# Optimization experiments

Measured on AMD Instinct MI355X. Metric: run time of the kernel, lower is better.

Reference implementation:

```python
import jax, jax.numpy as jnp
import numpy as np

B, N, E = 2, 50000, 1000000
F_IN, MSG, F_OUT, EDGE_F = 64, 64, 64, 16

def softsign(v):
    return v / (1.0 + jnp.abs(v))

def setup_inputs() -> dict:
    key = jax.random.key(0)
    ks = jax.random.split(key, 12)
    def w(k, i, o, s=0.02):
        return jax.random.normal(k, (i, o), jnp.float32) * s
    return dict(
        h=jax.random.normal(ks[0], (B, N, F_IN), jnp.float32),
        x=jax.random.normal(ks[1], (B, N, 4), jnp.float32),
        edge_index=jax.random.randint(ks[2], (2, E), 0, N),
        edge_attribute=jax.random.normal(ks[3], (B, E, EDGE_F), jnp.float32),
        w_e1=w(ks[4], 2 * F_IN + 1 + EDGE_F, MSG), b_e1=jnp.zeros((MSG,), jnp.float32),
        w_e2=w(ks[5], MSG, MSG), b_e2=jnp.zeros((MSG,), jnp.float32),
        w_f1=w(ks[6], F_IN + MSG, MSG), b_f1=jnp.zeros((MSG,), jnp.float32),
        w_f2=w(ks[7], MSG, F_OUT), b_f2=jnp.zeros((F_OUT,), jnp.float32),
        w_c1=w(ks[8], MSG, MSG), b_c1=jnp.zeros((MSG,), jnp.float32),
        w_c2=w(ks[9], MSG, 1, 0.001),  # xavier gain=0.001, no bias
        self_mult=jnp.asarray(0.7, jnp.float32),
        other_mult=jnp.asarray(-0.3, jnp.float32),
    )

def reference(h, x, edge_index, edge_attribute, w_e1, b_e1, w_e2, b_e2,
              w_f1, b_f1, w_f2, b_f2, w_c1, b_c1, w_c2, self_mult, other_mult):
    row, col = edge_index[0], edge_index[1]
    n = h.shape[1]
    # radials: Minkowski distance^2 with metric (-,+,+,+)
    diff = x[:, row] - x[:, col]                     # [B,E,4]
    sq = diff * diff
    radial = (jnp.sum(sq, axis=-1) - 2.0 * sq[..., 0])[..., None]  # [B,E,1]
    # edge MLP -> messages m_ij
    m_in = jnp.concatenate([h[:, row], h[:, col], radial, edge_attribute], axis=-1)
    m = jax.nn.silu(m_in @ w_e1 + b_e1)
    m = softsign(m @ w_e2 + b_e2)                    # [B,E,MSG]
    # coordinate update
    phi = jax.nn.silu(m @ w_c1 + b_c1) @ w_c2        # [B,E,1]
    lin = self_mult * x[:, row] + other_mult * x[:, col]
    weighted = lin * phi                             # [B,E,4]
    seg = lambda d: jax.vmap(lambda dd: jax.ops.segment_sum(dd, row, num_segments=n))(d)
    count = jnp.zeros((n,), jnp.float32).at[row].add(1.0)
    count = jnp.maximum(count, 1.0)[None, :, None]   # clamp(min=1)
    x_updated = x + seg(weighted) / count            # segment mean
    # feature update
    agg = seg(m)                                     # [B,N,MSG] segment sum
    f_in = jnp.concatenate([h, agg], axis=-1)
    h_updated = softsign(jax.nn.silu(f_in @ w_f1 + b_f1) @ w_f2 + b_f2)
    return h_updated, x_updated
```

## Files before the change

### kernel.cpp

```cpp
#include <hip/hip_runtime.h>
#include <hip/hip_bf16.h>
#include <cstdint>
#include <cstddef>

#define NN 50000
#define EE 1000000
#define NB 2
#define OUT_ELEMS (NB * NN * 64 + NB * NN * 4)

#define MSTR 72
#define TILE (32 * MSTR)

#define P_E1 0
#define P_E2 10240
#define P_C1 14336
#define P_F1 18432
#define P_F2 26624
#define E1_MAIN_SHORTS 8192

#define WS_CNT   0
#define WS_OFF   200704
#define WS_CUR   401408
#define WS_PART  602112
#define WS_ECS   603136
#define WS_PK    16603136
#define WS_HB    16664576
#define WS_LIN   29464576

#define NPART 196

typedef __attribute__((ext_vector_type(8))) short short8;
typedef __attribute__((ext_vector_type(4))) float f32x4;

__device__ __forceinline__ float fast_rcp(float v) { return __builtin_amdgcn_rcpf(v); }
__device__ __forceinline__ float silu_f(float v) { return v * fast_rcp(1.0f + __expf(-v)); }
__device__ __forceinline__ float ssgn_f(float v) { return v * fast_rcp(1.0f + fabsf(v)); }

__device__ __forceinline__ short f2bf(float f) {
    __hip_bfloat16 h = __float2bfloat16(f);
    return *reinterpret_cast<short*>(&h);
}
__device__ __forceinline__ float bf2f(short s) {
    union { unsigned u; float f; } c; c.u = ((unsigned)(unsigned short)s) << 16; return c.f;
}
__device__ __forceinline__ short8 pack8(float4 a, float4 b) {
    short8 r;
    r[0] = f2bf(a.x); r[1] = f2bf(a.y); r[2] = f2bf(a.z); r[3] = f2bf(a.w);
    r[4] = f2bf(b.x); r[5] = f2bf(b.y); r[6] = f2bf(b.z); r[7] = f2bf(b.w);
    return r;
}

#define PREP_CONV 3125
#define PREP_PACK 15
#define PREP_HIST 3907
#define PREP_ZERO 3321

__global__ void prep_kernel(const float* __restrict__ h, short* __restrict__ hb16,
                            const float* __restrict__ w_e1, const float* __restrict__ w_e2,
                            const float* __restrict__ w_c1, const float* __restrict__ w_f1,
                            const float* __restrict__ w_f2, short* __restrict__ pk,
                            const int* __restrict__ ei, int* __restrict__ cnt_i,
                            float* __restrict__ out)
{
    const int bid = blockIdx.x;
    if (bid < PREP_CONV) {
        size_t i = ((size_t)bid * 256 + threadIdx.x) * 8;
        float4 lo = *reinterpret_cast<const float4*>(h + i);
        float4 hi = *reinterpret_cast<const float4*>(h + i + 4);
        *reinterpret_cast<short8*>(hb16 + i) = pack8(lo, hi);
    } else if (bid < PREP_CONV + PREP_PACK) {
        int g = (bid - PREP_CONV) * 256 + threadIdx.x;
        const int G_E1 = 5 * 4 * 64, G_E2 = 2 * 4 * 64, G_C1 = 2 * 4 * 64;
        const int G_F1 = 4 * 4 * 64, G_F2 = 2 * 4 * 64;
        if (g >= G_E1 + G_E2 + G_C1 + G_F1 + G_F2) return;
        const float* W; int loc; int mat;
        if (g < G_E1)                        { W = w_e1; loc = g;                         mat = 0; }
        else if (g < G_E1+G_E2)              { W = w_e2; loc = g - G_E1;                  mat = 1; }
        else if (g < G_E1+G_E2+G_C1)         { W = w_c1; loc = g - G_E1 - G_E2;           mat = 2; }
        else if (g < G_E1+G_E2+G_C1+G_F1)    { W = w_f1; loc = g - G_E1 - G_E2 - G_C1;    mat = 3; }
        else                                 { W = w_f2; loc = g - G_E1-G_E2-G_C1-G_F1;   mat = 4; }
        int l = loc & 63, n = (loc >> 6) & 3, s = loc >> 8;
        short8 out8;
        #pragma unroll
        for (int j = 0; j < 8; j++) {
            int kp = s * 32 + ((l >> 4) * 8) + j;
            int ko; bool valid;
            if (mat == 0) {
                if (kp < 128)      { ko = kp;     valid = true; }
                else if (kp < 144) { ko = kp + 1; valid = true; }
                else if (kp == 144){ ko = 128;    valid = true; }
                else               { ko = 0;      valid = false; }
            } else if (mat == 3) { ko = kp; valid = kp < 128; }
            else                 { ko = kp; valid = kp < 64; }
            float v = valid ? W[ko * 64 + (n * 16 + (l & 15))] : 0.0f;
            out8[j] = f2bf(v);
        }
        *reinterpret_cast<short8*>(pk + (size_t)g * 8) = out8;
    } else if (bid < PREP_CONV + PREP_PACK + PREP_HIST) {
        int e = (bid - PREP_CONV - PREP_PACK) * 256 + threadIdx.x;
        if (e < EE) atomicAdd(&cnt_i[ei[e]], 1);
    } else {
        size_t i = ((size_t)(bid - PREP_CONV - PREP_PACK - PREP_HIST) * 256 + threadIdx.x) * 8;
        if (i < OUT_ELEMS) {
            float4 z = float4{0, 0, 0, 0};
            *reinterpret_cast<float4*>(out + i)     = z;
            *reinterpret_cast<float4*>(out + i + 4) = z;
        }
    }
}

__global__ void scanA(const int* __restrict__ cnt_i, int* __restrict__ part) {
    int i = blockIdx.x * 256 + threadIdx.x;
    int v = (i < NN) ? cnt_i[i] : 0;
    #pragma unroll
    for (int d = 1; d < 64; d <<= 1) v += __shfl_xor(v, d);
    __shared__ int red[4];
    if ((threadIdx.x & 63) == 0) red[threadIdx.x >> 6] = v;
    __syncthreads();
    if (threadIdx.x == 0) part[blockIdx.x] = red[0] + red[1] + red[2] + red[3];
}

__global__ void scanB(int* __restrict__ part) {
    __shared__ int s[256];
    int t = threadIdx.x;
    int v = (t < NPART) ? part[t] : 0;
    s[t] = v;
    __syncthreads();
    for (int d = 1; d < 256; d <<= 1) {
        int u = (t >= d) ? s[t - d] : 0;
        __syncthreads();
        s[t] += u;
        __syncthreads();
    }
    if (t < NPART) part[t] = s[t] - v;
}

__global__ void scanC(const int* __restrict__ cnt_i, const int* __restrict__ part,
                      int* __restrict__ off, int* __restrict__ cur) {
    __shared__ int s[256];
    int i = blockIdx.x * 256 + threadIdx.x;
    int t = threadIdx.x;
    int v = (i < NN) ? cnt_i[i] : 0;
    s[t] = v;
    __syncthreads();
    for (int d = 1; d < 256; d <<= 1) {
        int u = (t >= d) ? s[t - d] : 0;
        __syncthreads();
        s[t] += u;
        __syncthreads();
    }
    int excl = s[t] - v + part[blockIdx.x];
    if (i < NN) { off[i] = excl; cur[i] = excl; }
    if (i == 0) off[NN] = EE;
}

__global__ void scatter_kernel(const int* __restrict__ ei, const float* __restrict__ x,
                               const float* __restrict__ sm_p, const float* __restrict__ om_p,
                               int* __restrict__ cur, int4* __restrict__ ecs,
                               short* __restrict__ lins) {
    int e = blockIdx.x * 256 + threadIdx.x;
    if (e >= EE) return;
    int r = ei[e], c = ei[EE + e];
    int p = atomicAdd(&cur[r], 1);
    const float smv = sm_p[0], omv = om_p[0];
    short rp[2];
    short8 lv;
    #pragma unroll
    for (int b = 0; b < 2; b++) {
        float4 xr = *reinterpret_cast<const float4*>(x + ((size_t)b * NN + r) * 4);
        float4 xc = *reinterpret_cast<const float4*>(x + ((size_t)b * NN + c) * 4);
        float d0 = xr.x - xc.x, d1 = xr.y - xc.y, d2 = xr.z - xc.z, d3 = xr.w - xc.w;
        rp[b] = f2bf(d1 * d1 + d2 * d2 + d3 * d3 - d0 * d0);
        lv[b * 4 + 0] = f2bf(smv * xr.x + omv * xc.x);
        lv[b * 4 + 1] = f2bf(smv * xr.y + omv * xc.y);
        lv[b * 4 + 2] = f2bf(smv * xr.z + omv * xc.z);
        lv[b * 4 + 3] = f2bf(smv * xr.w + omv * xc.w);
    }
    int radpair = (int)(unsigned short)rp[0] | ((int)(unsigned short)rp[1] << 16);
    ecs[p] = make_int4(e, r, c, radpair);
    *reinterpret_cast<short8*>(lins + (size_t)p * 8) = lv;
}

__global__ __launch_bounds__(256, 3) void edge_kernel(
    const short* __restrict__ hb16,
    const float* __restrict__ ea, const int4* __restrict__ ecs,
    const short* __restrict__ lins,
    const float* __restrict__ b_e1, const float* __restrict__ b_e2,
    const float* __restrict__ b_c1, const float* __restrict__ w_c2,
    const short* __restrict__ pk,
    float* __restrict__ agg, float* __restrict__ xagg)
{
    __shared__ short wlds[E1_MAIN_SHORTS];
    __shared__ short smem[4][2 * TILE];
    const int wid  = threadIdx.x >> 6;
    const int lane = threadIdx.x & 63;
    short* sm  = smem[wid];
    float* smf = reinterpret_cast<float*>(sm);

    {
        short8* dst = reinterpret_cast<short8*>(wlds);
        const short8* src = reinterpret_cast<const short8*>(pk);
        #pragma unroll
        for (int i = 0; i < E1_MAIN_SHORTS / 8 / 256; i++)
            dst[i * 256 + threadIdx.x] = src[i * 256 + threadIdx.x];
    }
    __syncthreads();

    const int nwg = gridDim.x;
    const int q = nwg >> 3, r_ = nwg & 7;
    const int xcd = blockIdx.x & 7, kk = blockIdx.x >> 3;
    const int bswz = (xcd < r_ ? xcd * (q + 1) : r_ * (q + 1) + (xcd - r_) * q) + kk;

    const int WPB = EE / 32;
    const int gw = bswz * 4 + wid;
    if (gw >= WPB) return;
    const int i0 = gw * 32;

    const int l15 = lane & 15;
    const int gq  = lane >> 4;
    const int kg  = gq * 8;

    int eid = 0, row = 0, col = 0, radpair = 0;
    short8 lv = short8{0, 0, 0, 0, 0, 0, 0, 0};
    if (lane < 32) {
        int4 ec = ecs[i0 + lane];
        eid = ec.x; row = ec.y; col = ec.z; radpair = ec.w;
        lv = *reinterpret_cast<const short8*>(lins + (size_t)(i0 + lane) * 8);
    }

    int rowm[2], colm[2], eidm[2], radpm[2];
    #pragma unroll
    for (int m = 0; m < 2; m++) {
        int src = m * 16 + l15;
        rowm[m] = __shfl(row, src);
        colm[m] = __shfl(col, src);
        eidm[m] = __shfl(eid, src);
        radpm[m] = __shfl(radpair, src);
    }
    const short* hbb[2] = { hb16, hb16 + (size_t)NN * 64 };
    const short8* pke1L = reinterpret_cast<const short8*>(wlds);
    const short8* pke1G = reinterpret_cast<const short8*>(pk + P_E1);
    const short8* pke2  = reinterpret_cast<const short8*>(pk + P_E2);
    const short8* pkc1  = reinterpret_cast<const short8*>(pk + P_C1);

    short8 tail[2][2];
    #pragma unroll
    for (int b = 0; b < 2; b++)
        #pragma unroll
        for (int m = 0; m < 2; m++) {
            short8 v = short8{0, 0, 0, 0, 0, 0, 0, 0};
            if (gq < 2) {
                const float* src = ea + ((size_t)b * EE + eidm[m]) * 16 + gq * 8;
                float4 lo = *reinterpret_cast<const float4*>(src);
                float4 hi = *reinterpret_cast<const float4*>(src + 4);
                v = pack8(lo, hi);
            } else if (gq == 2) {
                v[0] = (short)((b == 0) ? (radpm[m] & 0xffff) : ((unsigned)radpm[m] >> 16));
            }
            tail[b][m] = v;
        }

    f32x4 acc[2][2][4];
    #pragma unroll
    for (int n = 0; n < 4; n++) {
        float bias = b_e1[n * 16 + l15];
        #pragma unroll
        for (int b = 0; b < 2; b++)
            #pragma unroll
            for (int m = 0; m < 2; m++) acc[b][m][n] = f32x4{bias, bias, bias, bias};
    }
    __builtin_amdgcn_s_setprio(1);
    #pragma unroll
    for (int n = 0; n < 4; n++) {
        short8 bfr = pke1G[(4 * 4 + n) * 64 + lane];
        #pragma unroll
        for (int b = 0; b < 2; b++)
            #pragma unroll
            for (int m = 0; m < 2; m++)
                acc[b][m][n] = __builtin_amdgcn_mfma_f32_16x16x32_bf16(tail[b][m], bfr, acc[b][m][n], 0, 0, 0);
    }
    __builtin_amdgcn_s_setprio(0);
    #pragma unroll
    for (int s = 0; s < 2; s++) {
        short8 afr[2][2];
        #pragma unroll
        for (int b = 0; b < 2; b++)
            #pragma unroll
            for (int m = 0; m < 2; m++)
                afr[b][m] = *reinterpret_cast<const short8*>(
                    hbb[b] + (size_t)rowm[m] * 64 + s * 32 + kg);
        __builtin_amdgcn_s_setprio(1);
        #pragma unroll
        for (int n = 0; n < 4; n++) {
            short8 bfr = pke1L[(s * 4 + n) * 64 + lane];
            #pragma unroll
            for (int b = 0; b < 2; b++)
                #pragma unroll
                for (int m = 0; m < 2; m++)
                    acc[b][m][n] = __builtin_amdgcn_mfma_f32_16x16x32_bf16(afr[b][m], bfr, acc[b][m][n], 0, 0, 0);
        }
        __builtin_amdgcn_s_setprio(0);
    }
    #pragma unroll
    for (int s2 = 0; s2 < 2; s2++) {
        short8 afr[2][2];
        #pragma unroll
        for (int b = 0; b < 2; b++)
            #pragma unroll
            for (int m = 0; m < 2; m++)
                afr[b][m] = *reinterpret_cast<const short8*>(
                    hbb[b] + (size_t)colm[m] * 64 + s2 * 32 + kg);
        __builtin_amdgcn_s_setprio(1);
        #pragma unroll
        for (int n = 0; n < 4; n++) {
            short8 bfr = pke1L[((2 + s2) * 4 + n) * 64 + lane];
            #pragma unroll
            for (int b = 0; b < 2; b++)
                #pragma unroll
                for (int m = 0; m < 2; m++)
                    acc[b][m][n] = __builtin_amdgcn_mfma_f32_16x16x32_bf16(afr[b][m], bfr, acc[b][m][n], 0, 0, 0);
        }
        __builtin_amdgcn_s_setprio(0);
    }

    #pragma unroll
    for (int b = 0; b < 2; b++)
        #pragma unroll
        for (int m = 0; m < 2; m++)
            #pragma unroll
            for (int n = 0; n < 4; n++)
                #pragma unroll
                for (int r = 0; r < 4; r++)
                    sm[b * TILE + (m * 16 + gq * 4 + r) * MSTR + n * 16 + l15] =
                        f2bf(silu_f(acc[b][m][n][r]));
    asm volatile("s_waitcnt lgkmcnt(0)" ::: "memory");

    f32x4 acc2[2][2][4];
    #pragma unroll
    for (int n = 0; n < 4; n++) {
        float bias = b_e2[n * 16 + l15];
        #pragma unroll
        for (int b = 0; b < 2; b++)
            #pragma unroll
            for (int m = 0; m < 2; m++) acc2[b][m][n] = f32x4{bias, bias, bias, bias};
    }
    #pragma unroll
    for (int s = 0; s < 2; s++) {
        short8 afr[2][2];
        #pragma unroll
        for (int b = 0; b < 2; b++)
            #pragma unroll
            for (int m = 0; m < 2; m++)
                afr[b][m] = *reinterpret_cast<const short8*>(
                    sm + b * TILE + (m * 16 + l15) * MSTR + s * 32 + kg);
        __builtin_amdgcn_s_setprio(1);
        #pragma unroll
        for (int n = 0; n < 4; n++) {
            short8 bfr = pke2[(s * 4 + n) * 64 + lane];
            #pragma unroll
            for (int b = 0; b < 2; b++)
                #pragma unroll
                for (int m = 0; m < 2; m++)
                    acc2[b][m][n] = __builtin_amdgcn_mfma_f32_16x16x32_bf16(afr[b][m], bfr, acc2[b][m][n], 0, 0, 0);
        }
        __builtin_amdgcn_s_setprio(0);
    }
    asm volatile("s_waitcnt lgkmcnt(0)" ::: "memory");

    #pragma unroll
    for (int b = 0; b < 2; b++)
        #pragma unroll
        for (int m = 0; m < 2; m++)
            #pragma unroll
            for (int n = 0; n < 4; n++)
                #pragma unroll
                for (int r = 0; r < 4; r++)
                    sm[b * TILE + (m * 16 + gq * 4 + r) * MSTR + n * 16 + l15] =
                        f2bf(ssgn_f(acc2[b][m][n][r]));
    asm volatile("s_waitcnt lgkmcnt(0)" ::: "memory");

    f32x4 acc3[2][2][4];
    #pragma unroll
    for (int n = 0; n < 4; n++) {
        float bias = b_c1[n * 16 + l15];
        #pragma unroll
        for (int b = 0; b < 2; b++)
            #pragma unroll
            for (int m = 0; m < 2; m++) acc3[b][m][n] = f32x4{bias, bias, bias, bias};
    }
    #pragma unroll
    for (int s = 0; s < 2; s++) {
        short8 afr[2][2];
        #pragma unroll
        for (int b = 0; b < 2; b++)
            #pragma unroll
            for (int m = 0; m < 2; m++)
                afr[b][m] = *reinterpret_cast<const short8*>(
                    sm + b * TILE + (m * 16 + l15) * MSTR + s * 32 + kg);
        __builtin_amdgcn_s_setprio(1);
        #pragma unroll
        for (int n = 0; n < 4; n++) {
            short8 bfr = pkc1[(s * 4 + n) * 64 + lane];
            #pragma unroll
            for (int b = 0; b < 2; b++)
                #pragma unroll
                for (int m = 0; m < 2; m++)
                    acc3[b][m][n] = __builtin_amdgcn_mfma_f32_16x16x32_bf16(afr[b][m], bfr, acc3[b][m][n], 0, 0, 0);
        }
        __builtin_amdgcn_s_setprio(0);
    }
    float wc2v[4];
    #pragma unroll
    for (int n = 0; n < 4; n++) wc2v[n] = w_c2[n * 16 + l15];
    #pragma unroll
    for (int b = 0; b < 2; b++)
        #pragma unroll
        for (int m = 0; m < 2; m++)
            #pragma unroll
            for (int r = 0; r < 4; r++) {
                float v = 0.0f;
                #pragma unroll
                for (int n = 0; n < 4; n++) v = fmaf(silu_f(acc3[b][m][n][r]), wc2v[n], v);
                v += __shfl_xor(v, 1); v += __shfl_xor(v, 2);
                v += __shfl_xor(v, 4); v += __shfl_xor(v, 8);
                if (l15 == 0) smf[b * (TILE / 2) + (m * 16 + gq * 4 + r) * 36 + 32] = v;
            }
    asm volatile("s_waitcnt lgkmcnt(0)" ::: "memory");

    if (lane < 32) {
        float phi0 = smf[lane * 36 + 32];
        float phi1 = smf[(TILE / 2) + lane * 36 + 32];
        float4 wv0, wv1;
        wv0.x = bf2f(lv[0]) * phi0; wv0.y = bf2f(lv[1]) * phi0;
        wv0.z = bf2f(lv[2]) * phi0; wv0.w = bf2f(lv[3]) * phi0;
        wv1.x = bf2f(lv[4]) * phi1; wv1.y = bf2f(lv[5]) * phi1;
        wv1.z = bf2f(lv[6]) * phi1; wv1.w = bf2f(lv[7]) * phi1;
        *reinterpret_cast<float4*>(smf + lane * 36 + 32) = wv0;
        *reinterpret_cast<float4*>(smf + (TILE / 2) + lane * 36 + 32) = wv1;
    }
    asm volatile("s_waitcnt lgkmcnt(0)" ::: "memory");

    int nrow = __shfl_down(row, 1);
    unsigned long long bmask = __ballot((lane == 31) || (lane < 31 && row != nrow));
    float* aggb0 = agg;
    float* aggb1 = agg + (size_t)NN * 64;
    float* xb    = xagg + (size_t)((lane >> 2) & 1) * NN * 4;
    const int xsel = ((lane >> 2) & 1) * (TILE / 2) + (lane & 3);
    float mv0 = 0.0f, mv1 = 0.0f, xv = 0.0f;
    #pragma unroll
    for (int e = 0; e < 32; e++) {
        mv0 += bf2f(sm[e * MSTR + lane]);
        mv1 += bf2f(sm[TILE + e * MSTR + lane]);
        float t = smf[e * 36 + 32 + xsel];
        xv += (lane < 8) ? t : 0.0f;
        if ((bmask >> e) & 1ull) {
            int re = __shfl(row, e);
            atomicAdd(aggb0 + (size_t)re * 64 + lane, mv0);
            atomicAdd(aggb1 + (size_t)re * 64 + lane, mv1);
            if (lane < 8) atomicAdd(xb + (size_t)re * 4 + (lane & 3), xv);
            mv0 = 0.0f; mv1 = 0.0f; xv = 0.0f;
        }
    }
}

__global__ __launch_bounds__(256, 4) void node_kernel(
    const short* __restrict__ hb16, const float* __restrict__ x,
    const float* __restrict__ b_f1, const float* __restrict__ b_f2,
    const short* __restrict__ pk,
    const int* __restrict__ off,
    float* out_h, float* out_x)
{
    __shared__ short smem[4][32 * MSTR];
    const int wid  = threadIdx.x >> 6;
    const int lane = threadIdx.x & 63;
    short* sm = smem[wid];

    const int WN = (NN + 31) / 32;
    const int gw = blockIdx.x * 4 + wid;
    if (gw >= NB * WN) return;
    const int b  = gw / WN;
    const int n0 = (gw - b * WN) * 32;

    const int l15 = lane & 15;
    const int gq  = lane >> 4;
    const int kg  = gq * 8;

    const short* hbb  = hb16 + (size_t)b * NN * 64;
    const float* aggb = out_h + (size_t)b * NN * 64;

    f32x4 acc[2][4];
    #pragma unroll
    for (int n = 0; n < 4; n++) {
        float bias = b_f1[n * 16 + l15];
        #pragma unroll
        for (int m = 0; m < 2; m++) acc[m][n] = f32x4{bias, bias, bias, bias};
    }
    const short8* pkf1 = reinterpret_cast<const short8*>(pk + P_F1);
    #pragma unroll
    for (int s = 0; s < 4; s++) {
        short8 afr[2];
        #pragma unroll
        for (int m = 0; m < 2; m++) {
            int nd = n0 + m * 16 + l15;
            if (nd >= NN) nd = NN - 1;
            if (s < 2) {
                afr[m] = *reinterpret_cast<const short8*>(
                    hbb + (size_t)nd * 64 + s * 32 + kg);
            } else {
                const float* base = aggb + (size_t)nd * 64 + (s & 1) * 32 + kg;
                float4 lo = *reinterpret_cast<const float4*>(base);
                float4 hi = *reinterpret_cast<const float4*>(base + 4);
                afr[m] = pack8(lo, hi);
            }
        }
        __builtin_amdgcn_s_setprio(1);
        #pragma unroll
        for (int n = 0; n < 4; n++) {
            short8 bfr = pkf1[(s * 4 + n) * 64 + lane];
            #pragma unroll
            for (int m = 0; m < 2; m++)
                acc[m][n] = __builtin_amdgcn_mfma_f32_16x16x32_bf16(afr[m], bfr, acc[m][n], 0, 0, 0);
        }
        __builtin_amdgcn_s_setprio(0);
    }

    #pragma unroll
    for (int m = 0; m < 2; m++)
        #pragma unroll
        for (int n = 0; n < 4; n++)
            #pragma unroll
            for (int r = 0; r < 4; r++)
                sm[(m * 16 + gq * 4 + r) * MSTR + n * 16 + l15] = f2bf(silu_f(acc[m][n][r]));
    asm volatile("s_waitcnt lgkmcnt(0)" ::: "memory");

    f32x4 acc2[2][4];
    #pragma unroll
    for (int n = 0; n < 4; n++) {
        float bias = b_f2[n * 16 + l15];
        #pragma unroll
        for (int m = 0; m < 2; m++) acc2[m][n] = f32x4{bias, bias, bias, bias};
    }
    const short8* pkf2 = reinterpret_cast<const short8*>(pk + P_F2);
    #pragma unroll
    for (int s = 0; s < 2; s++) {
        short8 afr[2];
        #pragma unroll
        for (int m = 0; m < 2; m++)
            afr[m] = *reinterpret_cast<const short8*>(sm + (m * 16 + l15) * MSTR + s * 32 + kg);
        __builtin_amdgcn_s_setprio(1);
        #pragma unroll
        for (int n = 0; n < 4; n++) {
            short8 bfr = pkf2[(s * 4 + n) * 64 + lane];
            #pragma unroll
            for (int m = 0; m < 2; m++)
                acc2[m][n] = __builtin_amdgcn_mfma_f32_16x16x32_bf16(afr[m], bfr, acc2[m][n], 0, 0, 0);
        }
        __builtin_amdgcn_s_setprio(0);
    }

    float* ohb = out_h + (size_t)b * NN * 64;
    #pragma unroll
    for (int m = 0; m < 2; m++)
        #pragma unroll
        for (int r = 0; r < 4; r++) {
            int nd = n0 + m * 16 + gq * 4 + r;
            if (nd < NN) {
                #pragma unroll
                for (int n = 0; n < 4; n++)
                    ohb[(size_t)nd * 64 + n * 16 + l15] = ssgn_f(acc2[m][n][r]);
            }
        }

    const int node = n0 + lane;
    if (lane < 32 && node < NN) {
        int c_i = off[node + 1] - off[node];
        float c = (float)(c_i < 1 ? 1 : c_i);
        float invc = fast_rcp(c);
        const float4 xv = *reinterpret_cast<const float4*>(x + ((size_t)b * NN + node) * 4);
        float* xop = out_x + ((size_t)b * NN + node) * 4;
        float4 xa = *reinterpret_cast<float4*>(xop);
        float4 r;
        r.x = xv.x + xa.x * invc;
        r.y = xv.y + xa.y * invc;
        r.z = xv.z + xa.z * invc;
        r.w = xv.w + xa.w * invc;
        *reinterpret_cast<float4*>(xop) = r;
    }
}

extern "C" void kernel_launch(void* const* d_in, const int* in_sizes, int n_in,
                              void* d_out, int out_size, void* d_ws, size_t ws_size,
                              hipStream_t stream) {
    const float* h    = (const float*)d_in[0];
    const float* x    = (const float*)d_in[1];
    const int*   ei   = (const int*)d_in[2];
    const float* ea   = (const float*)d_in[3];
    const float* w_e1 = (const float*)d_in[4];
    const float* b_e1 = (const float*)d_in[5];
    const float* w_e2 = (const float*)d_in[6];
    const float* b_e2 = (const float*)d_in[7];
    const float* w_f1 = (const float*)d_in[8];
    const float* b_f1 = (const float*)d_in[9];
    const float* w_f2 = (const float*)d_in[10];
    const float* b_f2 = (const float*)d_in[11];
    const float* w_c1 = (const float*)d_in[12];
    const float* b_c1 = (const float*)d_in[13];
    const float* w_c2 = (const float*)d_in[14];
    const float* smp  = (const float*)d_in[15];
    const float* omp  = (const float*)d_in[16];

    float* out   = (float*)d_out;
    float* agg   = out;
    float* out_x = out + (size_t)NB * NN * 64;

    char* ws = (char*)d_ws;
    int*   cnt_i = (int*)(ws + WS_CNT);
    int*   off   = (int*)(ws + WS_OFF);
    int*   cur   = (int*)(ws + WS_CUR);
    int*   part  = (int*)(ws + WS_PART);
    int4*  ecs   = (int4*)(ws + WS_ECS);
    short* pk    = (short*)(ws + WS_PK);
    short* hb16  = (short*)(ws + WS_HB);
    short* lins  = (short*)(ws + WS_LIN);

    hipMemsetAsync(cnt_i, 0, (size_t)NN * sizeof(int), stream);

    prep_kernel<<<PREP_CONV + PREP_PACK + PREP_HIST + PREP_ZERO, 256, 0, stream>>>(
        h, hb16, w_e1, w_e2, w_c1, w_f1, w_f2, pk, ei, cnt_i, out);
    scanA<<<NPART, 256, 0, stream>>>(cnt_i, part);
    scanB<<<1, 256, 0, stream>>>(part);
    scanC<<<NPART, 256, 0, stream>>>(cnt_i, part, off, cur);
    scatter_kernel<<<(EE + 255) / 256, 256, 0, stream>>>(ei, x, smp, omp, cur, ecs, lins);

    const int edge_waves = EE / 32;
    const int edge_blocks = (edge_waves + 3) / 4;
    edge_kernel<<<edge_blocks, 256, 0, stream>>>(
        hb16, ea, ecs, lins, b_e1, b_e2, b_c1, w_c2, pk, agg, out_x);

    const int node_waves = NB * ((NN + 31) / 32);
    const int node_blocks = (node_waves + 3) / 4;
    node_kernel<<<node_blocks, 256, 0, stream>>>(
        hb16, x, b_f1, b_f2, pk, off, agg, out_x);
}
```

Measured before the change: 332.1 us.

## Make edge kernel persistent with software-prefetched next window of edge data

The edge kernel now launches a fixed grid of 768 blocks, and each wave loops over a contiguous range of 32-edge windows instead of handling a single window. Inside the loop it prefetches the next window's edge descriptors, coordinate data and column-node feature gathers while the current window's MLP runs. This hides gather latency and amortizes the per-block weight load into shared memory. In exchange it holds more registers for the prefetched fragments, and a fixed grid size may not match occupancy or balance well across CUs.

```diff
diff --git a/kernel.cpp b/kernel.cpp
--- a/kernel.cpp
+++ b/kernel.cpp
@@ -28,6 +28,9 @@
 #define WS_LIN   29464576
 
 #define NPART 196
+#define EDGE_BLOCKS 768
+#define TOTWAVE (EDGE_BLOCKS * 4)
+#define NWIN (EE / 32)
 
 typedef __attribute__((ext_vector_type(8))) short short8;
 typedef __attribute__((ext_vector_type(4))) float f32x4;
@@ -206,260 +209,293 @@
     }
     __syncthreads();
 
-    const int nwg = gridDim.x;
-    const int q = nwg >> 3, r_ = nwg & 7;
-    const int xcd = blockIdx.x & 7, kk = blockIdx.x >> 3;
-    const int bswz = (xcd < r_ ? xcd * (q + 1) : r_ * (q + 1) + (xcd - r_) * q) + kk;
-
-    const int WPB = EE / 32;
-    const int gw = bswz * 4 + wid;
-    if (gw >= WPB) return;
-    const int i0 = gw * 32;
+    const int bswz = (blockIdx.x & 7) * (EDGE_BLOCKS / 8) + (blockIdx.x >> 3);
+    const int gwave = bswz * 4 + wid;
+    const int wbeg = (int)(((long long)gwave * NWIN) / TOTWAVE);
+    const int wend = (int)(((long long)(gwave + 1) * NWIN) / TOTWAVE);
 
     const int l15 = lane & 15;
     const int gq  = lane >> 4;
     const int kg  = gq * 8;
 
-    int eid = 0, row = 0, col = 0, radpair = 0;
-    short8 lv = short8{0, 0, 0, 0, 0, 0, 0, 0};
-    if (lane < 32) {
-        int4 ec = ecs[i0 + lane];
-        eid = ec.x; row = ec.y; col = ec.z; radpair = ec.w;
-        lv = *reinterpret_cast<const short8*>(lins + (size_t)(i0 + lane) * 8);
-    }
-
-    int rowm[2], colm[2], eidm[2], radpm[2];
-    #pragma unroll
-    for (int m = 0; m < 2; m++) {
-        int src = m * 16 + l15;
-        rowm[m] = __shfl(row, src);
-        colm[m] = __shfl(col, src);
-        eidm[m] = __shfl(eid, src);
-        radpm[m] = __shfl(radpair, src);
-    }
     const short* hbb[2] = { hb16, hb16 + (size_t)NN * 64 };
     const short8* pke1L = reinterpret_cast<const short8*>(wlds);
     const short8* pke1G = reinterpret_cast<const short8*>(pk + P_E1);
     const short8* pke2  = reinterpret_cast<const short8*>(pk + P_E2);
     const short8* pkc1  = reinterpret_cast<const short8*>(pk + P_C1);
 
-    short8 tail[2][2];
-    #pragma unroll
-    for (int b = 0; b < 2; b++)
+    float wc2v[4];
+    #pragma unroll
+    for (int n = 0; n < 4; n++) wc2v[n] = w_c2[n * 16 + l15];
+
+    int4 ecC = make_int4(0, 0, 0, 0);
+    short8 lvC = short8{0, 0, 0, 0, 0, 0, 0, 0};
+    if (lane < 32) {
+        ecC = ecs[(size_t)wbeg * 32 + lane];
+        lvC = *reinterpret_cast<const short8*>(lins + ((size_t)wbeg * 32 + lane) * 8);
+    }
+    short8 colf[2][2][2];
+    {
+        int colm0[2];
+        #pragma unroll
+        for (int m = 0; m < 2; m++) colm0[m] = __shfl(ecC.z, m * 16 + l15);
+        #pragma unroll
+        for (int s2 = 0; s2 < 2; s2++)
+            #pragma unroll
+            for (int b = 0; b < 2; b++)
+                #pragma unroll
+                for (int m = 0; m < 2; m++)
+                    colf[s2][b][m] = *reinterpret_cast<const short8*>(
+                        hbb[b] + (size_t)colm0[m] * 64 + s2 * 32 + kg);
+    }
+
+    #pragma unroll 1
+    for (int w = wbeg; w < wend; w++) {
+        const bool hasN = (w + 1 < wend);
+
+        int4 ecN = make_int4(0, 0, 0, 0);
+        short8 lvN = short8{0, 0, 0, 0, 0, 0, 0, 0};
+        if (hasN && lane < 32) {
+            ecN = ecs[(size_t)(w + 1) * 32 + lane];
+            lvN = *reinterpret_cast<const short8*>(lins + ((size_t)(w + 1) * 32 + lane) * 8);
+        }
+
+        int rowm[2], eidm[2], radpm[2];
         #pragma unroll
         for (int m = 0; m < 2; m++) {
-            short8 v = short8{0, 0, 0, 0, 0, 0, 0, 0};
-            if (gq < 2) {
-                const float* src = ea + ((size_t)b * EE + eidm[m]) * 16 + gq * 8;
-                float4 lo = *reinterpret_cast<const float4*>(src);
-                float4 hi = *reinterpret_cast<const float4*>(src + 4);
-                v = pack8(lo, hi);
-            } else if (gq == 2) {
-                v[0] = (short)((b == 0) ? (radpm[m] & 0xffff) : ((unsigned)radpm[m] >> 16));
-            }
-            tail[b][m] = v;
-        }
-
-    f32x4 acc[2][2][4];
-    #pragma unroll
-    for (int n = 0; n < 4; n++) {
-        float bias = b_e1[n * 16 + l15];
+            int src = m * 16 + l15;
+            rowm[m]  = __shfl(ecC.y, src);
+            eidm[m]  = __shfl(ecC.x, src);
+            radpm[m] = __shfl(ecC.w, src);
+        }
+
+        short8 tail[2][2];
         #pragma unroll
         for (int b = 0; b < 2; b++)
             #pragma unroll
-            for (int m = 0; m < 2; m++) acc[b][m][n] = f32x4{bias, bias, bias, bias};
-    }
-    __builtin_amdgcn_s_setprio(1);
-    #pragma unroll
-    for (int n = 0; n < 4; n++) {
-        short8 bfr = pke1G[(4 * 4 + n) * 64 + lane];
+            for (int m = 0; m < 2; m++) {
+                short8 v = short8{0, 0, 0, 0, 0, 0, 0, 0};
+                if (gq < 2) {
+                    const float* src = ea + ((size_t)b * EE + eidm[m]) * 16 + gq * 8;
+                    float4 lo = *reinterpret_cast<const float4*>(src);
+                    float4 hi = *reinterpret_cast<const float4*>(src + 4);
+                    v = pack8(lo, hi);
+                } else if (gq == 2) {
+                    v[0] = (short)((b == 0) ? (radpm[m] & 0xffff)
+                                            : ((unsigned)radpm[m] >> 16));
+                }
+                tail[b][m] = v;
+            }
+
+        f32x4 acc[2][2][4];
+        #pragma unroll
+        for (int n = 0; n < 4; n++) {
+            float bias = b_e1[n * 16 + l15];
+            #pragma unroll
+            for (int b = 0; b < 2; b++)
+                #pragma unroll
+                for (int m = 0; m < 2; m++) acc[b][m][n] = f32x4{bias, bias, bias, bias};
+        }
+        __builtin_amdgcn_s_setprio(1);
+        #pragma unroll
+        for (int n = 0; n < 4; n++) {
+            short8 bfr = pke1G[(4 * 4 + n) * 64 + lane];
+            #pragma unroll
+            for (int b = 0; b < 2; b++)
+                #pragma unroll
+                for (int m = 0; m < 2; m++)
+                    acc[b][m][n] = __builtin_amdgcn_mfma_f32_16x16x32_bf16(tail[b][m], bfr, acc[b][m][n], 0, 0, 0);
+        }
+        __builtin_amdgcn_s_setprio(0);
+        #pragma unroll
+        for (int s = 0; s < 2; s++) {
+            short8 afr[2][2];
+            #pragma unroll
+            for (int b = 0; b < 2; b++)
+                #pragma unroll
+                for (int m = 0; m < 2; m++)
+                    afr[b][m] = *reinterpret_cast<const short8*>(
+                        hbb[b] + (size_t)rowm[m] * 64 + s * 32 + kg);
+            __builtin_amdgcn_s_setprio(1);
+            #pragma unroll
+            for (int n = 0; n < 4; n++) {
+                short8 bfr = pke1L[(s * 4 + n) * 64 + lane];
+                #pragma unroll
+                for (int b = 0; b < 2; b++)
+                    #pragma unroll
+                    for (int m = 0; m < 2; m++)
+                        acc[b][m][n] = __builtin_amdgcn_mfma_f32_16x16x32_bf16(afr[b][m], bfr, acc[b][m][n], 0, 0, 0);
+            }
+            __builtin_amdgcn_s_setprio(0);
+        }
+        __builtin_amdgcn_s_setprio(1);
+        #pragma unroll
+        for (int s2 = 0; s2 < 2; s2++)
+            #pragma unroll
+            for (int n = 0; n < 4; n++) {
+                short8 bfr = pke1L[((2 + s2) * 4 + n) * 64 + lane];
+                #pragma unroll
+                for (int b = 0; b < 2; b++)
+                    #pragma unroll
+                    for (int m = 0; m < 2; m++)
+                        acc[b][m][n] = __builtin_amdgcn_mfma_f32_16x16x32_bf16(colf[s2][b][m], bfr, acc[b][m][n], 0, 0, 0);
+            }
+        __builtin_amdgcn_s_setprio(0);
+
+        if (hasN) {
+            int colmN[2];
+            #pragma unroll
+            for (int m = 0; m < 2; m++) colmN[m] = __shfl(ecN.z, m * 16 + l15);
+            #pragma unroll
+            for (int s2 = 0; s2 < 2; s2++)
+                #pragma unroll
+                for (int b = 0; b < 2; b++)
+                    #pragma unroll
+                    for (int m = 0; m < 2; m++)
+                        colf[s2][b][m] = *reinterpret_cast<const short8*>(
+                            hbb[b] + (size_t)colmN[m] * 64 + s2 * 32 + kg);
+        }
+
         #pragma unroll
         for (int b = 0; b < 2; b++)
             #pragma unroll
             for (int m = 0; m < 2; m++)
-                acc[b][m][n] = __builtin_amdgcn_mfma_f32_16x16x32_bf16(tail[b][m], bfr, acc[b][m][n], 0, 0, 0);
-    }
-    __builtin_amdgcn_s_setprio(0);
-    #pragma unroll
-    for (int s = 0; s < 2; s++) {
-        short8 afr[2][2];
+                #pragma unroll
+                for (int n = 0; n < 4; n++)
+                    #pragma unroll
+                    for (int r = 0; r < 4; r++)
+                        sm[b * TILE + (m * 16 + gq * 4 + r) * MSTR + n * 16 + l15] =
+                            f2bf(silu_f(acc[b][m][n][r]));
+        asm volatile("s_waitcnt lgkmcnt(0)" ::: "memory");
+
+        f32x4 acc2[2][2][4];
+        #pragma unroll
+        for (int n = 0; n < 4; n++) {
+            float bias = b_e2[n * 16 + l15];
+            #pragma unroll
+            for (int b = 0; b < 2; b++)
+                #pragma unroll
+                for (int m = 0; m < 2; m++) acc2[b][m][n] = f32x4{bias, bias, bias, bias};
+        }
+        #pragma unroll
+        for (int s = 0; s < 2; s++) {
+            short8 afr[2][2];
+            #pragma unroll
+            for (int b = 0; b < 2; b++)
+                #pragma unroll
+                for (int m = 0; m < 2; m++)
+                    afr[b][m] = *reinterpret_cast<const short8*>(
+                        sm + b * TILE + (m * 16 + l15) * MSTR + s * 32 + kg);
+            __builtin_amdgcn_s_setprio(1);
+            #pragma unroll
+            for (int n = 0; n < 4; n++) {
+                short8 bfr = pke2[(s * 4 + n) * 64 + lane];
+                #pragma unroll
+                for (int b = 0; b < 2; b++)
+                    #pragma unroll
+                    for (int m = 0; m < 2; m++)
+                        acc2[b][m][n] = __builtin_amdgcn_mfma_f32_16x16x32_bf16(afr[b][m], bfr, acc2[b][m][n], 0, 0, 0);
+            }
+            __builtin_amdgcn_s_setprio(0);
+        }
+        asm volatile("s_waitcnt lgkmcnt(0)" ::: "memory");
+
         #pragma unroll
         for (int b = 0; b < 2; b++)
             #pragma unroll
             for (int m = 0; m < 2; m++)
-                afr[b][m] = *reinterpret_cast<const short8*>(
-                    hbb[b] + (size_t)rowm[m] * 64 + s * 32 + kg);
-        __builtin_amdgcn_s_setprio(1);
+                #pragma unroll
+                for (int n = 0; n < 4; n++)
+                    #pragma unroll
+                    for (int r = 0; r < 4; r++)
+                        sm[b * TILE + (m * 16 + gq * 4 + r) * MSTR + n * 16 + l15] =
+                            f2bf(ssgn_f(acc2[b][m][n][r]));
+        asm volatile("s_waitcnt lgkmcnt(0)" ::: "memory");
+
+        f32x4 acc3[2][2][4];
         #pragma unroll
         for (int n = 0; n < 4; n++) {
-            short8 bfr = pke1L[(s * 4 + n) * 64 + lane];
+            float bias = b_c1[n * 16 + l15];
+            #pragma unroll
+            for (int b = 0; b < 2; b++)
+                #pragma unroll
+                for (int m = 0; m < 2; m++) acc3[b][m][n] = f32x4{bias, bias, bias, bias};
+        }
+        #pragma unroll
+        for (int s = 0; s < 2; s++) {
+            short8 afr[2][2];
             #pragma unroll
             for (int b = 0; b < 2; b++)
                 #pragma unroll
                 for (int m = 0; m < 2; m++)
-                    acc[b][m][n] = __builtin_amdgcn_mfma_f32_16x16x32_bf16(afr[b][m], bfr, acc[b][m][n], 0, 0, 0);
-        }
-        __builtin_amdgcn_s_setprio(0);
-    }
-    #pragma unroll
-    for (int s2 = 0; s2 < 2; s2++) {
-        short8 afr[2][2];
+                    afr[b][m] = *reinterpret_cast<const short8*>(
+                        sm + b * TILE + (m * 16 + l15) * MSTR + s * 32 + kg);
+            __builtin_amdgcn_s_setprio(1);
+            #pragma unroll
+            for (int n = 0; n < 4; n++) {
+                short8 bfr = pkc1[(s * 4 + n) * 64 + lane];
+                #pragma unroll
+                for (int b = 0; b < 2; b++)
+                    #pragma unroll
+                    for (int m = 0; m < 2; m++)
+                        acc3[b][m][n] = __builtin_amdgcn_mfma_f32_16x16x32_bf16(afr[b][m], bfr, acc3[b][m][n], 0, 0, 0);
+            }
+            __builtin_amdgcn_s_setprio(0);
+        }
         #pragma unroll
         for (int b = 0; b < 2; b++)
             #pragma unroll
             for (int m = 0; m < 2; m++)
-                afr[b][m] = *reinterpret_cast<const short8*>(
-                    hbb[b] + (size_t)colm[m] * 64 + s2 * 32 + kg);
-        __builtin_amdgcn_s_setprio(1);
-        #pragma unroll
-        for (int n = 0; n < 4; n++) {
-            short8 bfr = pke1L[((2 + s2) * 4 + n) * 64 + lane];
-            #pragma unroll
-            for (int b = 0; b < 2; b++)
-                #pragma unroll
-                for (int m = 0; m < 2; m++)
-                    acc[b][m][n] = __builtin_amdgcn_mfma_f32_16x16x32_bf16(afr[b][m], bfr, acc[b][m][n], 0, 0, 0);
-        }
-        __builtin_amdgcn_s_setprio(0);
-    }
-
-    #pragma unroll
-    for (int b = 0; b < 2; b++)
-        #pragma unroll
-        for (int m = 0; m < 2; m++)
-            #pragma unroll
-            for (int n = 0; n < 4; n++)
-                #pragma unroll
-                for (int r = 0; r < 4; r++)
-                    sm[b * TILE + (m * 16 + gq * 4 + r) * MSTR + n * 16 + l15] =
-                        f2bf(silu_f(acc[b][m][n][r]));
-    asm volatile("s_waitcnt lgkmcnt(0)" ::: "memory");
-
-    f32x4 acc2[2][2][4];
-    #pragma unroll
-    for (int n = 0; n < 4; n++) {
-        float bias = b_e2[n * 16 + l15];
-        #pragma unroll
-        for (int b = 0; b < 2; b++)
-            #pragma unroll
-            for (int m = 0; m < 2; m++) acc2[b][m][n] = f32x4{bias, bias, bias, bias};
-    }
-    #pragma unroll
-    for (int s = 0; s < 2; s++) {
-        short8 afr[2][2];
-        #pragma unroll
-        for (int b = 0; b < 2; b++)
-            #pragma unroll
-            for (int m = 0; m < 2; m++)
-                afr[b][m] = *reinterpret_cast<const short8*>(
-                    sm + b * TILE + (m * 16 + l15) * MSTR + s * 32 + kg);
-        __builtin_amdgcn_s_setprio(1);
-        #pragma unroll
-        for (int n = 0; n < 4; n++) {
-            short8 bfr = pke2[(s * 4 + n) * 64 + lane];
-            #pragma unroll
-            for (int b = 0; b < 2; b++)
-                #pragma unroll
-                for (int m = 0; m < 2; m++)
-                    acc2[b][m][n] = __builtin_amdgcn_mfma_f32_16x16x32_bf16(afr[b][m], bfr, acc2[b][m][n], 0, 0, 0);
-        }
-        __builtin_amdgcn_s_setprio(0);
-    }
-    asm volatile("s_waitcnt lgkmcnt(0)" ::: "memory");
-
-    #pragma unroll
-    for (int b = 0; b < 2; b++)
-        #pragma unroll
-        for (int m = 0; m < 2; m++)
-            #pragma unroll
-            for (int n = 0; n < 4; n++)
-                #pragma unroll
-                for (int r = 0; r < 4; r++)
-                    sm[b * TILE + (m * 16 + gq * 4 + r) * MSTR + n * 16 + l15] =
-                        f2bf(ssgn_f(acc2[b][m][n][r]));
-    asm volatile("s_waitcnt lgkmcnt(0)" ::: "memory");
-
-    f32x4 acc3[2][2][4];
-    #pragma unroll
-    for (int n = 0; n < 4; n++) {
-        float bias = b_c1[n * 16 + l15];
-        #pragma unroll
-        for (int b = 0; b < 2; b++)
-            #pragma unroll
-            for (int m = 0; m < 2; m++) acc3[b][m][n] = f32x4{bias, bias, bias, bias};
-    }
-    #pragma unroll
-    for (int s = 0; s < 2; s++) {
-        short8 afr[2][2];
-        #pragma unroll
-        for (int b = 0; b < 2; b++)
-            #pragma unroll
-            for (int m = 0; m < 2; m++)
-                afr[b][m] = *reinterpret_cast<const short8*>(
-                    sm + b * TILE + (m * 16 + l15) * MSTR + s * 32 + kg);
-        __builtin_amdgcn_s_setprio(1);
-        #pragma unroll
-        for (int n = 0; n < 4; n++) {
-            short8 bfr = pkc1[(s * 4 + n) * 64 + lane];
-            #pragma unroll
-            for (int b = 0; b < 2; b++)
-                #pragma unroll
-                for (int m = 0; m < 2; m++)
-                    acc3[b][m][n] = __builtin_amdgcn_mfma_f32_16x16x32_bf16(afr[b][m], bfr, acc3[b][m][n], 0, 0, 0);
-        }
-        __builtin_amdgcn_s_setprio(0);
-    }
-    float wc2v[4];
-    #pragma unroll
-    for (int n = 0; n < 4; n++) wc2v[n] = w_c2[n * 16 + l15];
-    #pragma unroll
-    for (int b = 0; b < 2; b++)
-        #pragma unroll
-        for (int m = 0; m < 2; m++)
-            #pragma unroll
-            for (int r = 0; r < 4; r++) {
-                float v = 0.0f;
-                #pragma unroll
-                for (int n = 0; n < 4; n++) v = fmaf(silu_f(acc3[b][m][n][r]), wc2v[n], v);
-                v += __shfl_xor(v, 1); v += __shfl_xor(v, 2);
-                v += __shfl_xor(v, 4); v += __shfl_xor(v, 8);
-                if (l15 == 0) smf[b * (TILE / 2) + (m * 16 + gq * 4 + r) * 36 + 32] = v;
-            }
-    asm volatile("s_waitcnt lgkmcnt(0)" ::: "memory");
-
-    if (lane < 32) {
-        float phi0 = smf[lane * 36 + 32];
-        float phi1 = smf[(TILE / 2) + lane * 36 + 32];
-        float4 wv0, wv1;
-        wv0.x = bf2f(lv[0]) * phi0; wv0.y = bf2f(lv[1]) * phi0;
-        wv0.z = bf2f(lv[2]) * phi0; wv0.w = bf2f(lv[3]) * phi0;
-        wv1.x = bf2f(lv[4]) * phi1; wv1.y = bf2f(lv[5]) * phi1;
-        wv1.z = bf2f(lv[6]) * phi1; wv1.w = bf2f(lv[7]) * phi1;
-        *reinterpret_cast<float4*>(smf + lane * 36 + 32) = wv0;
-        *reinterpret_cast<float4*>(smf + (TILE / 2) + lane * 36 + 32) = wv1;
-    }
-    asm volatile("s_waitcnt lgkmcnt(0)" ::: "memory");
-
-    int nrow = __shfl_down(row, 1);
-    unsigned long long bmask = __ballot((lane == 31) || (lane < 31 && row != nrow));
-    float* aggb0 = agg;
-    float* aggb1 = agg + (size_t)NN * 64;
-    float* xb    = xagg + (size_t)((lane >> 2) & 1) * NN * 4;
-    const int xsel = ((lane >> 2) & 1) * (TILE / 2) + (lane & 3);
-    float mv0 = 0.0f, mv1 = 0.0f, xv = 0.0f;
-    #pragma unroll
-    for (int e = 0; e < 32; e++) {
-        mv0 += bf2f(sm[e * MSTR + lane]);
-        mv1 += bf2f(sm[TILE + e * MSTR + lane]);
-        float t = smf[e * 36 + 32 + xsel];
-        xv += (lane < 8) ? t : 0.0f;
-        if ((bmask >> e) & 1ull) {
-            int re = __shfl(row, e);
-            atomicAdd(aggb0 + (size_t)re * 64 + lane, mv0);
-            atomicAdd(aggb1 + (size_t)re * 64 + lane, mv1);
-            if (lane < 8) atomicAdd(xb + (size_t)re * 4 + (lane & 3), xv);
-            mv0 = 0.0f; mv1 = 0.0f; xv = 0.0f;
-        }
+                #pragma unroll
+                for (int r = 0; r < 4; r++) {
+                    float v = 0.0f;
+                    #pragma unroll
+                    for (int n = 0; n < 4; n++) v = fmaf(silu_f(acc3[b][m][n][r]), wc2v[n], v);
+                    v += __shfl_xor(v, 1); v += __shfl_xor(v, 2);
+                    v += __shfl_xor(v, 4); v += __shfl_xor(v, 8);
+                    if (l15 == 0) smf[b * (TILE / 2) + (m * 16 + gq * 4 + r) * 36 + 32] = v;
+                }
+        asm volatile("s_waitcnt lgkmcnt(0)" ::: "memory");
+
+        if (lane < 32) {
+            float phi0 = smf[lane * 36 + 32];
+            float phi1 = smf[(TILE / 2) + lane * 36 + 32];
+            float4 wv0, wv1;
+            wv0.x = bf2f(lvC[0]) * phi0; wv0.y = bf2f(lvC[1]) * phi0;
+            wv0.z = bf2f(lvC[2]) * phi0; wv0.w = bf2f(lvC[3]) * phi0;
+            wv1.x = bf2f(lvC[4]) * phi1; wv1.y = bf2f(lvC[5]) * phi1;
+            wv1.z = bf2f(lvC[6]) * phi1; wv1.w = bf2f(lvC[7]) * phi1;
+            *reinterpret_cast<float4*>(smf + lane * 36 + 32) = wv0;
+            *reinterpret_cast<float4*>(smf + (TILE / 2) + lane * 36 + 32) = wv1;
+        }
+        asm volatile("s_waitcnt lgkmcnt(0)" ::: "memory");
+
+        const int rowHere = ecC.y;
+        int nrow = __shfl_down(rowHere, 1);
+        unsigned long long bmask = __ballot((lane == 31) || (lane < 31 && rowHere != nrow));
+        float* aggb0 = agg;
+        float* aggb1 = agg + (size_t)NN * 64;
+        float* xb    = xagg + (size_t)((lane >> 2) & 1) * NN * 4;
+        const int xsel = ((lane >> 2) & 1) * (TILE / 2) + (lane & 3);
+        float mv0 = 0.0f, mv1 = 0.0f, xv = 0.0f;
+        #pragma unroll
+        for (int e = 0; e < 32; e++) {
+            mv0 += bf2f(sm[e * MSTR + lane]);
+            mv1 += bf2f(sm[TILE + e * MSTR + lane]);
+            float t = smf[e * 36 + 32 + xsel];
+            xv += (lane < 8) ? t : 0.0f;
+            if ((bmask >> e) & 1ull) {
+                int re = __shfl(rowHere, e);
+                atomicAdd(aggb0 + (size_t)re * 64 + lane, mv0);
+                atomicAdd(aggb1 + (size_t)re * 64 + lane, mv1);
+                if (lane < 8) atomicAdd(xb + (size_t)re * 4 + (lane & 3), xv);
+                mv0 = 0.0f; mv1 = 0.0f; xv = 0.0f;
+            }
+        }
+        asm volatile("s_waitcnt lgkmcnt(0)" ::: "memory");
+
+        ecC = ecN;
+        lvC = lvN;
     }
 }
 
@@ -632,9 +668,7 @@
     scanC<<<NPART, 256, 0, stream>>>(cnt_i, part, off, cur);
     scatter_kernel<<<(EE + 255) / 256, 256, 0, stream>>>(ei, x, smp, omp, cur, ecs, lins);
 
-    const int edge_waves = EE / 32;
-    const int edge_blocks = (edge_waves + 3) / 4;
-    edge_kernel<<<edge_blocks, 256, 0, stream>>>(
+    edge_kernel<<<EDGE_BLOCKS, 256, 0, stream>>>(
         hb16, ea, ecs, lins, b_e1, b_e2, b_c1, w_c2, pk, agg, out_x);
 
     const int node_waves = NB * ((NN + 31) / 32);
```

Result: slower. 529.0 us (+59.3%).
